# Kernel optimization log

Measured on AMD Instinct MI355X. Metric: run time of the kernel, lower is better.

The kernel has to match this reference:

```python
import jax, jax.numpy as jnp
import numpy as np

N_NODES = 50000


def _gcn_conv(x, edge_index, W, b):
    # PyG GCNConv (default flags): add self-loops, symmetric normalization,
    # linear transform, scatter-add aggregation, bias.
    N = x.shape[0]
    row, col = edge_index[0], edge_index[1]  # messages flow row -> col
    loop = jnp.arange(N)
    row_f = jnp.concatenate([row, loop])
    col_f = jnp.concatenate([col, loop])
    deg = jax.ops.segment_sum(jnp.ones(col_f.shape[0], dtype=x.dtype), col_f,
                              num_segments=N)
    deg_inv_sqrt = jnp.where(deg > 0, jax.lax.rsqrt(jnp.maximum(deg, 1e-12)), 0.0)
    norm = deg_inv_sqrt[row_f] * deg_inv_sqrt[col_f]  # [E+N]
    h = x @ W                                          # [N, out]
    msg = h[row_f] * norm[:, None]                     # gather + scale
    out = jax.ops.segment_sum(msg, col_f, num_segments=N)  # scatter-add
    return out + b


def setup_inputs() -> dict:
    key = jax.random.key(0)
    ks = jax.random.split(key, 6)
    d_in, d_hid, d_out = 128, 128, 64
    E = 800000
    x = jax.random.normal(ks[0], (N_NODES, d_in), dtype=jnp.float32)
    edge_index = jax.random.randint(ks[1], (2, E), 0, N_NODES, dtype=jnp.int64)
    edge_label = jax.random.uniform(ks[2], (100000,), dtype=jnp.float32)
    edge_label_index = jax.random.randint(ks[3], (2, 100000), 0, N_NODES,
                                          dtype=jnp.int64)
    # Glorot-style init for GCNConv linear weights
    W1 = jax.random.normal(ks[4], (d_in, d_hid), dtype=jnp.float32) / np.sqrt(d_in)
    b1 = jnp.zeros((d_hid,), dtype=jnp.float32)
    W2 = jax.random.normal(ks[5], (d_hid, d_out), dtype=jnp.float32) / np.sqrt(d_hid)
    b2 = jnp.zeros((d_out,), dtype=jnp.float32)
    return {"x": x, "edge_index": edge_index, "edge_label": edge_label,
            "edge_label_index": edge_label_index,
            "W1": W1, "b1": b1, "W2": W2, "b2": b2}


def reference(x, edge_index, edge_label, edge_label_index, W1, b1, W2, b2):
    h = jax.nn.relu(_gcn_conv(x, edge_index, W1, b1))
    # dropout is identity in eval mode (training=False)
    z = _gcn_conv(h, edge_index, W2, b2)
    return z
```

## Files before the change

kernel.cpp:

```cpp
#include <hip/hip_runtime.h>


typedef unsigned int u32;
typedef __attribute__((ext_vector_type(8))) short short8;
typedef __attribute__((ext_vector_type(4))) float floatx4;

static inline int cdiv_l(long a, int b) { return (int)((a + b - 1) / b); }

constexpr int NPB  = 512;
constexpr int EPB  = 4096;
constexpr int MAXB = 128;
constexpr int CAP  = 12288;

__device__ __forceinline__ u32 pack_bf16(float a, float b) {
  union { float f; u32 i; } ua, ub;
  ua.f = a; ub.f = b;
  u32 x = (ua.i + 0x7fffu + ((ua.i >> 16) & 1u)) >> 16;
  u32 y = (ub.i + 0x7fffu + ((ub.i >> 16) & 1u)) & 0xffff0000u;
  return x | y;
}

__device__ __forceinline__ short bf16r(float f) {
  union { float f; u32 i; } u; u.f = f;
  return (short)((u.i + 0x7fffu + ((u.i >> 16) & 1u)) >> 16);
}

__device__ __forceinline__ void add8(float* a, uint4 v) {
  union { u32 i; float f; } t;
  t.i = v.x << 16;         a[0] += t.f;
  t.i = v.x & 0xffff0000u; a[1] += t.f;
  t.i = v.y << 16;         a[2] += t.f;
  t.i = v.y & 0xffff0000u; a[3] += t.f;
  t.i = v.z << 16;         a[4] += t.f;
  t.i = v.z & 0xffff0000u; a[5] += t.f;
  t.i = v.w << 16;         a[6] += t.f;
  t.i = v.w & 0xffff0000u; a[7] += t.f;
}

__global__ __launch_bounds__(MAXB) void k_init(int* __restrict__ cur) {
  cur[threadIdx.x] = threadIdx.x * CAP;
}

__global__ __launch_bounds__(256) void k_part(const int* __restrict__ ei,
                                              int* __restrict__ cur,
                                              u32* __restrict__ ebuf, int E) {
  __shared__ int hist[MAXB];
  __shared__ int curs[MAXB];
  const int tid = threadIdx.x;
  const int* ecol = ei + E;
  if (tid < MAXB) hist[tid] = 0;
  __syncthreads();
  const int base = blockIdx.x * EPB;
#pragma unroll
  for (int j = 0; j < EPB / 256; ++j) {
    int e = base + j * 256 + tid;
    if (e < E) atomicAdd(hist + (ecol[e] >> 9), 1);
  }
  __syncthreads();
  if (tid < MAXB) {
    int n = hist[tid];
    curs[tid] = n ? atomicAdd(cur + tid, n) : 0;
  }
  __syncthreads();
#pragma unroll
  for (int j = 0; j < EPB / 256; ++j) {
    int e = base + j * 256 + tid;
    if (e < E) {
      int r = ei[e];
      int c = ecol[e];
      int b = c >> 9;
      int p = atomicAdd(curs + b, 1);
      if (p < (b + 1) * CAP)
        ebuf[p] = (u32)r | ((u32)(c & (NPB - 1)) << 16);
    }
  }
}

__global__ __launch_bounds__(NPB) void k_csr(const u32* __restrict__ ebuf,
                                             const int* __restrict__ cur,
                                             int* __restrict__ off,
                                             int* __restrict__ deg,
                                             float* __restrict__ dis,
                                             int* __restrict__ csr, int N) {
  __shared__ int cnt[NPB];
  __shared__ int curl[NPB];
  __shared__ int wsum[NPB / 64];
  const int tid = threadIdx.x;
  const int b = blockIdx.x;
  const int s = b * CAP;
  const int e = min(cur[b], s + CAP);
  cnt[tid] = 0;
  __syncthreads();
  for (int i = s + tid; i < e; i += NPB)
    atomicAdd(cnt + (ebuf[i] >> 16), 1);
  __syncthreads();
  const int lane = tid & 63, w = tid >> 6;
  int v = cnt[tid];
  int incl = v;
#pragma unroll
  for (int d = 1; d < 64; d <<= 1) {
    int x = __shfl_up(incl, d, 64);
    if (lane >= d) incl += x;
  }
  if (lane == 63) wsum[w] = incl;
  __syncthreads();
  if (w == 0 && lane < NPB / 64) {
    int sv = wsum[lane];
#pragma unroll
    for (int d = 1; d < NPB / 64; d <<= 1) {
      int x = __shfl_up(sv, d, 64);
      if (lane >= d) sv += x;
    }
    wsum[lane] = sv;
  }
  __syncthreads();
  int excl = ((w > 0) ? wsum[w - 1] : 0) + incl - v;
  int node = b * NPB + tid;
  if (node < N) {
    off[node] = s + excl;
    deg[node] = v;
    dis[node] = rsqrtf((float)v + 1.0f);
  }
  curl[tid] = excl;
  __syncthreads();
  for (int i = s + tid; i < e; i += NPB) {
    u32 pk = ebuf[i];
    int p = atomicAdd(curl + (pk >> 16), 1);
    csr[s + p] = (int)(pk & 0xffffu);
  }
}

template <int M>
__global__ __launch_bounds__(256) void k_gemm_mfma(
    const float* __restrict__ A, const float* __restrict__ W,
    const float* __restrict__ dis, u32* __restrict__ outp, int N) {
  constexpr int K = 128;
  constexpr int NC = M / 16;
  constexpr int LROW = 133;
  constexpr int W2 = M / 2;
  __shared__ float eb[4][16 * LROW];
  const int tid = threadIdx.x;
  const int w = tid >> 6, lane = tid & 63;
  const int quad = lane >> 4, n16 = lane & 15;
  const int row0 = (blockIdx.x * 4 + w) * 16;

  floatx4 acc[NC];
#pragma unroll
  for (int c = 0; c < NC; ++c) acc[c] = {0.f, 0.f, 0.f, 0.f};

  const int am = row0 + n16;
  const bool av = am < N;
  const float* arow = A + (long)am * K;

#pragma unroll
  for (int kc = 0; kc < 4; ++kc) {
    const int kb = kc * 32 + quad * 8;
    float4 a0 = make_float4(0.f, 0.f, 0.f, 0.f);
    float4 a1 = make_float4(0.f, 0.f, 0.f, 0.f);
    if (av) {
      a0 = *(const float4*)(arow + kb);
      a1 = *(const float4*)(arow + kb + 4);
    }
    short8 af;
    af[0] = bf16r(a0.x); af[1] = bf16r(a0.y); af[2] = bf16r(a0.z); af[3] = bf16r(a0.w);
    af[4] = bf16r(a1.x); af[5] = bf16r(a1.y); af[6] = bf16r(a1.z); af[7] = bf16r(a1.w);
    const float* wbase = W + (long)kb * M + n16;
#pragma unroll
    for (int c = 0; c < NC; ++c) {
      const float* wp = wbase + c * 16;
      short8 bf;
      bf[0] = bf16r(wp[0 * M]); bf[1] = bf16r(wp[1 * M]);
      bf[2] = bf16r(wp[2 * M]); bf[3] = bf16r(wp[3 * M]);
      bf[4] = bf16r(wp[4 * M]); bf[5] = bf16r(wp[5 * M]);
      bf[6] = bf16r(wp[6 * M]); bf[7] = bf16r(wp[7 * M]);
      acc[c] = __builtin_amdgcn_mfma_f32_16x16x32_bf16(af, bf, acc[c], 0, 0, 0);
    }
  }

  float dd[4];
#pragma unroll
  for (int r = 0; r < 4; ++r) {
    int rg = row0 + quad * 4 + r;
    dd[r] = (rg < N) ? dis[rg] : 0.f;
  }
  float* ep = eb[w];
#pragma unroll
  for (int c = 0; c < NC; ++c)
#pragma unroll
    for (int r = 0; r < 4; ++r)
      ep[(quad * 4 + r) * LROW + c * 16 + n16] = acc[c][r] * dd[r];
  __syncthreads();

#pragma unroll
  for (int i = 0; i < 16 * W2 / 64; ++i) {
    int idx = i * 64 + lane;
    int r = idx / W2, cp = idx % W2;
    int rg = row0 + r;
    if (rg < N) {
      u32 p = pack_bf16(ep[r * LROW + 2 * cp], ep[r * LROW + 2 * cp + 1]);
      outp[(long)rg * W2 + cp] = p;
    }
  }
}

__global__ __launch_bounds__(256) void k_gg(
    const uint4* __restrict__ hs, const int* __restrict__ off,
    const int* __restrict__ deg, const int* __restrict__ csr,
    const float* __restrict__ dis, const float* __restrict__ b1,
    const float* __restrict__ W2, u32* __restrict__ h2, int N) {
  constexpr int LG = 65;
  constexpr int LC = 66;
  __shared__ u32 lg[16 * LG];
  __shared__ float cb[16 * LC];
  const int tid = threadIdx.x;
  const int r = tid >> 4;
  const int lf = tid & 15;
  const int row0 = blockIdx.x * 16;
  const int n = row0 + r;

  u32 gw[4] = {0, 0, 0, 0};
  if (n < N) {
    const int s = off[n], e = s + deg[n];
    float acc[8] = {};
    add8(acc, hs[(long)n * 16 + lf]);
    int j = s;
    for (; j + 4 <= e; j += 4) {
      int s0 = csr[j], s1 = csr[j + 1], s2 = csr[j + 2], s3 = csr[j + 3];
      uint4 v0 = hs[(long)s0 * 16 + lf];
      uint4 v1 = hs[(long)s1 * 16 + lf];
      uint4 v2 = hs[(long)s2 * 16 + lf];
      uint4 v3 = hs[(long)s3 * 16 + lf];
      add8(acc, v0); add8(acc, v1); add8(acc, v2); add8(acc, v3);
    }
    for (; j < e; ++j) add8(acc, hs[(long)csr[j] * 16 + lf]);
    const float d = dis[n];
    const int f8 = lf * 8;
#pragma unroll
    for (int q = 0; q < 8; ++q)
      acc[q] = fmaxf(acc[q] * d + b1[f8 + q], 0.f);
#pragma unroll
    for (int q = 0; q < 4; ++q)
      gw[q] = pack_bf16(acc[2 * q], acc[2 * q + 1]);
  }
#pragma unroll
  for (int q = 0; q < 4; ++q) lg[r * LG + lf * 4 + q] = gw[q];
  __syncthreads();

  const int w = tid >> 6, lane = tid & 63;
  const int quad = lane >> 4, n16 = lane & 15;
  floatx4 acc4 = {0.f, 0.f, 0.f, 0.f};
#pragma unroll
  for (int kc = 0; kc < 4; ++kc) {
    const int kb = kc * 32 + quad * 8;
    const u32* ap = &lg[n16 * LG + (kb >> 1)];
    u32 aw[4] = {ap[0], ap[1], ap[2], ap[3]};
    short8 af = *(short8*)aw;
    const float* wp = W2 + (long)kb * 64 + w * 16 + n16;
    short8 bf;
    bf[0] = bf16r(wp[0 * 64]); bf[1] = bf16r(wp[1 * 64]);
    bf[2] = bf16r(wp[2 * 64]); bf[3] = bf16r(wp[3 * 64]);
    bf[4] = bf16r(wp[4 * 64]); bf[5] = bf16r(wp[5 * 64]);
    bf[6] = bf16r(wp[6 * 64]); bf[7] = bf16r(wp[7 * 64]);
    acc4 = __builtin_amdgcn_mfma_f32_16x16x32_bf16(af, bf, acc4, 0, 0, 0);
  }
  float dd[4];
#pragma unroll
  for (int r4 = 0; r4 < 4; ++r4) {
    int rg = row0 + quad * 4 + r4;
    dd[r4] = (rg < N) ? dis[rg] : 0.f;
  }
#pragma unroll
  for (int r4 = 0; r4 < 4; ++r4)
    cb[(quad * 4 + r4) * LC + w * 16 + n16] = acc4[r4] * dd[r4];
  __syncthreads();

#pragma unroll
  for (int i = 0; i < 2; ++i) {
    int idx = i * 256 + tid;
    int rr = idx >> 5, cw = idx & 31;
    int rg = row0 + rr;
    if (rg < N) {
      u32 p = pack_bf16(cb[rr * LC + 2 * cw], cb[rr * LC + 2 * cw + 1]);
      h2[(long)rg * 32 + cw] = p;
    }
  }
}

__global__ __launch_bounds__(256) void k_gather2(
    const uint4* __restrict__ hs, const int* __restrict__ off,
    const int* __restrict__ deg, const int* __restrict__ csr,
    const float* __restrict__ dis, const float* __restrict__ bias,
    float* __restrict__ out, int N) {
  constexpr int L = 8;
  const int local = threadIdx.x / L;
  const int lf = threadIdx.x % L;
  const int n = blockIdx.x * (256 / L) + local;
  if (n >= N) return;
  const int s = off[n], e = s + deg[n];
  float acc[8] = {};
  add8(acc, hs[(long)n * L + lf]);
  int j = s;
  for (; j + 4 <= e; j += 4) {
    int s0 = csr[j], s1 = csr[j + 1], s2 = csr[j + 2], s3 = csr[j + 3];
    uint4 v0 = hs[(long)s0 * L + lf];
    uint4 v1 = hs[(long)s1 * L + lf];
    uint4 v2 = hs[(long)s2 * L + lf];
    uint4 v3 = hs[(long)s3 * L + lf];
    add8(acc, v0); add8(acc, v1); add8(acc, v2); add8(acc, v3);
  }
  for (; j < e; ++j) add8(acc, hs[(long)csr[j] * L + lf]);
  const float d = dis[n];
  const int f8 = lf * 8;
  const float4 b0 = *(const float4*)(bias + f8);
  const float4 b1v = *(const float4*)(bias + f8 + 4);
  float4 o0, o1;
  o0.x = acc[0] * d + b0.x;
  o0.y = acc[1] * d + b0.y;
  o0.z = acc[2] * d + b0.z;
  o0.w = acc[3] * d + b0.w;
  o1.x = acc[4] * d + b1v.x;
  o1.y = acc[5] * d + b1v.y;
  o1.z = acc[6] * d + b1v.z;
  o1.w = acc[7] * d + b1v.w;
  *(float4*)(out + (long)n * 64 + f8) = o0;
  *(float4*)(out + (long)n * 64 + f8 + 4) = o1;
}

extern "C" void kernel_launch(void* const* d_in, const int* in_sizes, int n_in,
                              void* d_out, int out_size, void* d_ws, size_t ws_size,
                              hipStream_t stream) {
  const float* x  = (const float*)d_in[0];
  const int*   ei = (const int*)d_in[1];
  const float* W1 = (const float*)d_in[4];
  const float* b1 = (const float*)d_in[5];
  const float* W2 = (const float*)d_in[6];
  const float* b2 = (const float*)d_in[7];
  float* out = (float*)d_out;

  const int N = in_sizes[0] / 128;
  const int E = in_sizes[1] / 2;
  const int NBKT = cdiv_l(N, NPB);
  const int NBE  = cdiv_l(E, EPB);

  const long Np = (N + 64) & ~63L;
  const long BW = (long)NBKT * CAP;
  int*   cur  = (int*)d_ws;
  int*   off  = cur + 128;
  int*   deg  = off + Np;
  float* dis  = (float*)(deg + Np);
  u32*   ebuf = (u32*)(dis + Np);
  int*   csr  = (int*)(ebuf + BW);
  u32*   h    = (u32*)(csr + BW);
  u32*   h2   = h + (long)N * 64;

  k_init<<<1, MAXB, 0, stream>>>(cur);
  k_part<<<NBE, 256, 0, stream>>>(ei, cur, ebuf, E);
  k_csr<<<NBKT, NPB, 0, stream>>>(ebuf, cur, off, deg, dis, csr, N);

  k_gemm_mfma<128><<<cdiv_l(N, 64), 256, 0, stream>>>(x, W1, dis, h, N);

  k_gg<<<cdiv_l(N, 16), 256, 0, stream>>>((const uint4*)h, off, deg, csr,
                                          dis, b1, W2, h2, N);

  k_gather2<<<cdiv_l(N, 32), 256, 0, stream>>>((const uint4*)h2, off, deg, csr,
                                               dis, b2, out, N);
}
```

Baseline: 178.9 us.

## Fuse edge partition with first GEMM, move source norm into gather, shrink CSR

Runs the edge-bucketing pass and the first-layer X·W1 GEMM in one horizontally fused launch, so the two independent stages overlap and one launch disappears. Because the GEMM now runs before degrees exist, the per-source normalization is dropped from its epilogue and applied during the first-layer gather instead, which costs an extra dis load per edge. CSR source indices are stored as 16-bit values to halve index traffic, and the init kernel is replaced by a memset with bucket bases added at claim time. The 16-bit indices only hold while node ids fit in 16 bits, but N is 50000, so every node id fits and this is not a correctness issue for these inputs.

New measurement: 169.3 us. 1.06x faster.

```diff
diff --git a/kernel.cpp b/kernel.cpp
--- a/kernel.cpp
+++ b/kernel.cpp
@@ -2,6 +2,7 @@
 
 
 typedef unsigned int u32;
+typedef unsigned short ushort;
 typedef __attribute__((ext_vector_type(8))) short short8;
 typedef __attribute__((ext_vector_type(4))) float floatx4;
 
@@ -37,112 +38,63 @@
   t.i = v.w & 0xffff0000u; a[7] += t.f;
 }
 
-__global__ __launch_bounds__(MAXB) void k_init(int* __restrict__ cur) {
-  cur[threadIdx.x] = threadIdx.x * CAP;
-}
-
-__global__ __launch_bounds__(256) void k_part(const int* __restrict__ ei,
-                                              int* __restrict__ cur,
-                                              u32* __restrict__ ebuf, int E) {
+__device__ __forceinline__ void fma8(float* a, uint4 v, float s) {
+  union { u32 i; float f; } t;
+  t.i = v.x << 16;         a[0] += t.f * s;
+  t.i = v.x & 0xffff0000u; a[1] += t.f * s;
+  t.i = v.y << 16;         a[2] += t.f * s;
+  t.i = v.y & 0xffff0000u; a[3] += t.f * s;
+  t.i = v.z << 16;         a[4] += t.f * s;
+  t.i = v.z & 0xffff0000u; a[5] += t.f * s;
+  t.i = v.w << 16;         a[6] += t.f * s;
+  t.i = v.w & 0xffff0000u; a[7] += t.f * s;
+}
+
+__global__ __launch_bounds__(256) void k_fused1(
+    const int* __restrict__ ei, int* __restrict__ cur, u32* __restrict__ ebuf,
+    int E, int NBE,
+    const float* __restrict__ x, const float* __restrict__ W1,
+    u32* __restrict__ h, int N) {
+  __shared__ float eb[4][16 * 133];
   __shared__ int hist[MAXB];
   __shared__ int curs[MAXB];
   const int tid = threadIdx.x;
-  const int* ecol = ei + E;
-  if (tid < MAXB) hist[tid] = 0;
-  __syncthreads();
-  const int base = blockIdx.x * EPB;
-#pragma unroll
-  for (int j = 0; j < EPB / 256; ++j) {
-    int e = base + j * 256 + tid;
-    if (e < E) atomicAdd(hist + (ecol[e] >> 9), 1);
-  }
-  __syncthreads();
-  if (tid < MAXB) {
-    int n = hist[tid];
-    curs[tid] = n ? atomicAdd(cur + tid, n) : 0;
-  }
-  __syncthreads();
-#pragma unroll
-  for (int j = 0; j < EPB / 256; ++j) {
-    int e = base + j * 256 + tid;
-    if (e < E) {
-      int r = ei[e];
-      int c = ecol[e];
-      int b = c >> 9;
-      int p = atomicAdd(curs + b, 1);
-      if (p < (b + 1) * CAP)
-        ebuf[p] = (u32)r | ((u32)(c & (NPB - 1)) << 16);
-    }
-  }
-}
-
-__global__ __launch_bounds__(NPB) void k_csr(const u32* __restrict__ ebuf,
-                                             const int* __restrict__ cur,
-                                             int* __restrict__ off,
-                                             int* __restrict__ deg,
-                                             float* __restrict__ dis,
-                                             int* __restrict__ csr, int N) {
-  __shared__ int cnt[NPB];
-  __shared__ int curl[NPB];
-  __shared__ int wsum[NPB / 64];
-  const int tid = threadIdx.x;
-  const int b = blockIdx.x;
-  const int s = b * CAP;
-  const int e = min(cur[b], s + CAP);
-  cnt[tid] = 0;
-  __syncthreads();
-  for (int i = s + tid; i < e; i += NPB)
-    atomicAdd(cnt + (ebuf[i] >> 16), 1);
-  __syncthreads();
-  const int lane = tid & 63, w = tid >> 6;
-  int v = cnt[tid];
-  int incl = v;
-#pragma unroll
-  for (int d = 1; d < 64; d <<= 1) {
-    int x = __shfl_up(incl, d, 64);
-    if (lane >= d) incl += x;
-  }
-  if (lane == 63) wsum[w] = incl;
-  __syncthreads();
-  if (w == 0 && lane < NPB / 64) {
-    int sv = wsum[lane];
-#pragma unroll
-    for (int d = 1; d < NPB / 64; d <<= 1) {
-      int x = __shfl_up(sv, d, 64);
-      if (lane >= d) sv += x;
-    }
-    wsum[lane] = sv;
-  }
-  __syncthreads();
-  int excl = ((w > 0) ? wsum[w - 1] : 0) + incl - v;
-  int node = b * NPB + tid;
-  if (node < N) {
-    off[node] = s + excl;
-    deg[node] = v;
-    dis[node] = rsqrtf((float)v + 1.0f);
-  }
-  curl[tid] = excl;
-  __syncthreads();
-  for (int i = s + tid; i < e; i += NPB) {
-    u32 pk = ebuf[i];
-    int p = atomicAdd(curl + (pk >> 16), 1);
-    csr[s + p] = (int)(pk & 0xffffu);
-  }
-}
-
-template <int M>
-__global__ __launch_bounds__(256) void k_gemm_mfma(
-    const float* __restrict__ A, const float* __restrict__ W,
-    const float* __restrict__ dis, u32* __restrict__ outp, int N) {
-  constexpr int K = 128;
-  constexpr int NC = M / 16;
-  constexpr int LROW = 133;
-  constexpr int W2 = M / 2;
-  __shared__ float eb[4][16 * LROW];
-  const int tid = threadIdx.x;
+
+  if (blockIdx.x < (unsigned)NBE) {
+    const int* ecol = ei + E;
+    if (tid < MAXB) hist[tid] = 0;
+    __syncthreads();
+    const int base = blockIdx.x * EPB;
+#pragma unroll
+    for (int j = 0; j < EPB / 256; ++j) {
+      int e = base + j * 256 + tid;
+      if (e < E) atomicAdd(hist + (ecol[e] >> 9), 1);
+    }
+    __syncthreads();
+    if (tid < MAXB) {
+      int n = hist[tid];
+      curs[tid] = tid * CAP + (n ? atomicAdd(cur + tid, n) : 0);
+    }
+    __syncthreads();
+#pragma unroll
+    for (int j = 0; j < EPB / 256; ++j) {
+      int e = base + j * 256 + tid;
+      if (e < E) {
+        int r = ei[e];
+        int c = ecol[e];
+        int b = c >> 9;
+        int p = atomicAdd(curs + b, 1);
+        if (p < (b + 1) * CAP)
+          ebuf[p] = (u32)r | ((u32)(c & (NPB - 1)) << 16);
+      }
+    }
+    return;
+  }
+
+  constexpr int K = 128, M = 128, NC = 8, LROW = 133, WW = 64;
   const int w = tid >> 6, lane = tid & 63;
   const int quad = lane >> 4, n16 = lane & 15;
-  const int row0 = (blockIdx.x * 4 + w) * 16;
+  const int row0 = ((blockIdx.x - NBE) * 4 + w) * 16;
 
   floatx4 acc[NC];
 #pragma unroll
@@ -150,7 +102,7 @@
 
   const int am = row0 + n16;
   const bool av = am < N;
-  const float* arow = A + (long)am * K;
+  const float* arow = x + (long)am * K;
 
 #pragma unroll
   for (int kc = 0; kc < 4; ++kc) {
@@ -164,7 +116,7 @@
     short8 af;
     af[0] = bf16r(a0.x); af[1] = bf16r(a0.y); af[2] = bf16r(a0.z); af[3] = bf16r(a0.w);
     af[4] = bf16r(a1.x); af[5] = bf16r(a1.y); af[6] = bf16r(a1.z); af[7] = bf16r(a1.w);
-    const float* wbase = W + (long)kb * M + n16;
+    const float* wbase = W1 + (long)kb * M + n16;
 #pragma unroll
     for (int c = 0; c < NC; ++c) {
       const float* wp = wbase + c * 16;
@@ -177,35 +129,83 @@
     }
   }
 
-  float dd[4];
-#pragma unroll
-  for (int r = 0; r < 4; ++r) {
-    int rg = row0 + quad * 4 + r;
-    dd[r] = (rg < N) ? dis[rg] : 0.f;
-  }
   float* ep = eb[w];
 #pragma unroll
   for (int c = 0; c < NC; ++c)
 #pragma unroll
     for (int r = 0; r < 4; ++r)
-      ep[(quad * 4 + r) * LROW + c * 16 + n16] = acc[c][r] * dd[r];
-  __syncthreads();
-
-#pragma unroll
-  for (int i = 0; i < 16 * W2 / 64; ++i) {
+      ep[(quad * 4 + r) * LROW + c * 16 + n16] = acc[c][r];
+  __syncthreads();
+
+#pragma unroll
+  for (int i = 0; i < 16 * WW / 64; ++i) {
     int idx = i * 64 + lane;
-    int r = idx / W2, cp = idx % W2;
+    int r = idx / WW, cp = idx % WW;
     int rg = row0 + r;
     if (rg < N) {
       u32 p = pack_bf16(ep[r * LROW + 2 * cp], ep[r * LROW + 2 * cp + 1]);
-      outp[(long)rg * W2 + cp] = p;
-    }
+      h[(long)rg * WW + cp] = p;
+    }
+  }
+}
+
+__global__ __launch_bounds__(NPB) void k_csr(const u32* __restrict__ ebuf,
+                                             const int* __restrict__ cur,
+                                             int* __restrict__ off,
+                                             int* __restrict__ deg,
+                                             float* __restrict__ dis,
+                                             ushort* __restrict__ csr, int N) {
+  __shared__ int cnt[NPB];
+  __shared__ int curl[NPB];
+  __shared__ int wsum[NPB / 64];
+  const int tid = threadIdx.x;
+  const int b = blockIdx.x;
+  const int s = b * CAP;
+  const int e = s + min(cur[b], CAP);
+  cnt[tid] = 0;
+  __syncthreads();
+  for (int i = s + tid; i < e; i += NPB)
+    atomicAdd(cnt + (ebuf[i] >> 16), 1);
+  __syncthreads();
+  const int lane = tid & 63, w = tid >> 6;
+  int v = cnt[tid];
+  int incl = v;
+#pragma unroll
+  for (int d = 1; d < 64; d <<= 1) {
+    int x = __shfl_up(incl, d, 64);
+    if (lane >= d) incl += x;
+  }
+  if (lane == 63) wsum[w] = incl;
+  __syncthreads();
+  if (w == 0 && lane < NPB / 64) {
+    int sv = wsum[lane];
+#pragma unroll
+    for (int d = 1; d < NPB / 64; d <<= 1) {
+      int x = __shfl_up(sv, d, 64);
+      if (lane >= d) sv += x;
+    }
+    wsum[lane] = sv;
+  }
+  __syncthreads();
+  int excl = ((w > 0) ? wsum[w - 1] : 0) + incl - v;
+  int node = b * NPB + tid;
+  if (node < N) {
+    off[node] = s + excl;
+    deg[node] = v;
+    dis[node] = rsqrtf((float)v + 1.0f);
+  }
+  curl[tid] = excl;
+  __syncthreads();
+  for (int i = s + tid; i < e; i += NPB) {
+    u32 pk = ebuf[i];
+    int p = atomicAdd(curl + (pk >> 16), 1);
+    csr[s + p] = (ushort)(pk & 0xffffu);
   }
 }
 
 __global__ __launch_bounds__(256) void k_gg(
     const uint4* __restrict__ hs, const int* __restrict__ off,
-    const int* __restrict__ deg, const int* __restrict__ csr,
+    const int* __restrict__ deg, const ushort* __restrict__ csr,
     const float* __restrict__ dis, const float* __restrict__ b1,
     const float* __restrict__ W2, u32* __restrict__ h2, int N) {
   constexpr int LG = 65;
@@ -221,23 +221,27 @@
   u32 gw[4] = {0, 0, 0, 0};
   if (n < N) {
     const int s = off[n], e = s + deg[n];
+    const float dn = dis[n];
     float acc[8] = {};
-    add8(acc, hs[(long)n * 16 + lf]);
+    fma8(acc, hs[(long)n * 16 + lf], dn);
     int j = s;
     for (; j + 4 <= e; j += 4) {
       int s0 = csr[j], s1 = csr[j + 1], s2 = csr[j + 2], s3 = csr[j + 3];
+      float d0 = dis[s0], d1 = dis[s1], d2 = dis[s2], d3 = dis[s3];
       uint4 v0 = hs[(long)s0 * 16 + lf];
       uint4 v1 = hs[(long)s1 * 16 + lf];
       uint4 v2 = hs[(long)s2 * 16 + lf];
       uint4 v3 = hs[(long)s3 * 16 + lf];
-      add8(acc, v0); add8(acc, v1); add8(acc, v2); add8(acc, v3);
-    }
-    for (; j < e; ++j) add8(acc, hs[(long)csr[j] * 16 + lf]);
-    const float d = dis[n];
+      fma8(acc, v0, d0); fma8(acc, v1, d1); fma8(acc, v2, d2); fma8(acc, v3, d3);
+    }
+    for (; j < e; ++j) {
+      int s0 = csr[j];
+      fma8(acc, hs[(long)s0 * 16 + lf], dis[s0]);
+    }
     const int f8 = lf * 8;
 #pragma unroll
     for (int q = 0; q < 8; ++q)
-      acc[q] = fmaxf(acc[q] * d + b1[f8 + q], 0.f);
+      acc[q] = fmaxf(acc[q] * dn + b1[f8 + q], 0.f);
 #pragma unroll
     for (int q = 0; q < 4; ++q)
       gw[q] = pack_bf16(acc[2 * q], acc[2 * q + 1]);
@@ -288,7 +292,7 @@
 
 __global__ __launch_bounds__(256) void k_gather2(
     const uint4* __restrict__ hs, const int* __restrict__ off,
-    const int* __restrict__ deg, const int* __restrict__ csr,
+    const int* __restrict__ deg, const ushort* __restrict__ csr,
     const float* __restrict__ dis, const float* __restrict__ bias,
     float* __restrict__ out, int N) {
   constexpr int L = 8;
@@ -341,23 +345,24 @@
   const int E = in_sizes[1] / 2;
   const int NBKT = cdiv_l(N, NPB);
   const int NBE  = cdiv_l(E, EPB);
+  const int G1   = cdiv_l(N, 64);
 
   const long Np = (N + 64) & ~63L;
   const long BW = (long)NBKT * CAP;
-  int*   cur  = (int*)d_ws;
-  int*   off  = cur + 128;
-  int*   deg  = off + Np;
-  float* dis  = (float*)(deg + Np);
-  u32*   ebuf = (u32*)(dis + Np);
-  int*   csr  = (int*)(ebuf + BW);
-  u32*   h    = (u32*)(csr + BW);
-  u32*   h2   = h + (long)N * 64;
-
-  k_init<<<1, MAXB, 0, stream>>>(cur);
-  k_part<<<NBE, 256, 0, stream>>>(ei, cur, ebuf, E);
+  int*    cur  = (int*)d_ws;
+  int*    off  = cur + 128;
+  int*    deg  = off + Np;
+  float*  dis  = (float*)(deg + Np);
+  u32*    ebuf = (u32*)(dis + Np);
+  ushort* csr  = (ushort*)(ebuf + BW);
+  u32*    h    = (u32*)(csr + BW);
+  u32*    h2   = h + (long)N * 64;
+
+  hipMemsetAsync(cur, 0, MAXB * sizeof(int), stream);
+
+  k_fused1<<<NBE + G1, 256, 0, stream>>>(ei, cur, ebuf, E, NBE, x, W1, h, N);
+
   k_csr<<<NBKT, NPB, 0, stream>>>(ebuf, cur, off, deg, dis, csr, N);
-
-  k_gemm_mfma<128><<<cdiv_l(N, 64), 256, 0, stream>>>(x, W1, dis, h, N);
 
   k_gg<<<cdiv_l(N, 16), 256, 0, stream>>>((const uint4*)h, off, deg, csr,
                                           dis, b1, W2, h2, N);
```
